# Performance work log

Hardware: AMD Instinct MI355X
Metric: run time of the kernel (lower is better)

The kernel has to match this reference:

```python
import jax, jax.numpy as jnp
import numpy as np

MARGIN = 0.2
NEG_FLOOR = 0.6


def setup_inputs() -> dict:
    key = jax.random.key(0)
    k1, k2 = jax.random.split(key)
    inputs_col = jax.random.normal(k1, (8192, 128), dtype=jnp.float32)
    targets_col = jax.random.randint(k2, (8192,), 0, 512, dtype=jnp.int64)
    return {"inputs_col": inputs_col, "targets_col": targets_col}


def reference(inputs_col, targets_col):
    n = inputs_col.shape[0]
    sim = inputs_col @ inputs_col.T  # [n, n]

    same = targets_col[:, None] == targets_col[None, :]
    eye = jnp.eye(n, dtype=bool)
    pos_mask = same & ~eye
    neg_mask = ~same

    has_pos = jnp.any(pos_mask, axis=1)  # rows with at least one positive pair

    neg_inf = jnp.float32(-jnp.inf)
    max_pos = jnp.max(jnp.where(pos_mask, sim, neg_inf), axis=1)  # pos_pair_[-1]
    max_neg = jnp.max(jnp.where(neg_mask, sim, neg_inf), axis=1)  # neg_pair_[-1]

    # positives with sim < max_neg + margin
    sel_pos = pos_mask & (sim < (max_neg + MARGIN)[:, None])
    # negatives with sim > max(0.6, max_pos) - margin
    neg_thresh = jnp.maximum(jnp.float32(NEG_FLOOR), max_pos) - MARGIN
    sel_neg = neg_mask & (sim > neg_thresh[:, None])

    pos_loss = jnp.sum(jnp.where(sel_pos, 1.0 - sim, 0.0), axis=1)
    neg_loss = jnp.sum(jnp.where(sel_neg, sim, 0.0), axis=1)

    row_loss = jnp.where(has_pos, pos_loss + neg_loss, 0.0)
    loss = jnp.sum(row_loss) / n

    # rows that contributed at least one selected negative (and had positives)
    neg_count = jnp.sum((jnp.any(sel_neg, axis=1) & has_pos).astype(jnp.int32))
    return loss, neg_count
```

## Files before the change

### kernel.cpp

```cpp
#include <hip/hip_runtime.h>
#include <hip/hip_bf16.h>

#define NPTS 8192
#define DDIM 128
#define MARGIN 0.2f
#define NEG_FLOOR 0.6f
#define SENT -1e30f
#define NCHUNK 16
#define CHUNK (NPTS / NCHUNK)
#define BM 128
#define JT 64
#define NSTEP (CHUNK / JT)
#define NRB (NPTS / 256)

typedef __attribute__((ext_vector_type(8))) short short8;
typedef __attribute__((ext_vector_type(4))) float f32x4;
typedef __attribute__((ext_vector_type(4))) unsigned int uint4v;
typedef __attribute__((ext_vector_type(4))) unsigned short ushort4v;


__device__ __forceinline__ unsigned short f2bf(unsigned u) {
    return (unsigned short)((u + 0x7FFFu + ((u >> 16) & 1u)) >> 16);
}

__global__ __launch_bounds__(256) void k_convert(const uint4v* __restrict__ x,
                                                 ushort4v* __restrict__ xb) {
    int i = blockIdx.x * 256 + threadIdx.x;
    uint4v u = x[i];
    ushort4v o;
    o.x = f2bf(u.x); o.y = f2bf(u.y); o.z = f2bf(u.z); o.w = f2bf(u.w);
    xb[i] = o;
}

__device__ __forceinline__ void gload16(const unsigned char* g, unsigned char* l) {
    __builtin_amdgcn_global_load_lds(
        (const __attribute__((address_space(1))) unsigned int*)(const void*)g,
        (__attribute__((address_space(3))) unsigned int*)(void*)l, 16, 0, 0);
}


#define MFMA_PAIR(B_, cg0_)                                                           \
    short8 bA0 = *(const short8*)((B_) + (cg0_)*4096 + 0 * 1024 + lane * 16);         \
    short8 bA1 = *(const short8*)((B_) + (cg0_)*4096 + 1 * 1024 + lane * 16);         \
    short8 bA2 = *(const short8*)((B_) + (cg0_)*4096 + 2 * 1024 + lane * 16);         \
    short8 bA3 = *(const short8*)((B_) + (cg0_)*4096 + 3 * 1024 + lane * 16);         \
    short8 bB0 = *(const short8*)((B_) + (cg0_)*4096 + 4096 + 0 * 1024 + lane * 16);  \
    short8 bB1 = *(const short8*)((B_) + (cg0_)*4096 + 4096 + 1 * 1024 + lane * 16);  \
    short8 bB2 = *(const short8*)((B_) + (cg0_)*4096 + 4096 + 2 * 1024 + lane * 16);  \
    short8 bB3 = *(const short8*)((B_) + (cg0_)*4096 + 4096 + 3 * 1024 + lane * 16);  \
    f32x4 accA0 = {0.f,0.f,0.f,0.f}, accA1 = {0.f,0.f,0.f,0.f};                       \
    f32x4 accB0 = {0.f,0.f,0.f,0.f}, accB1 = {0.f,0.f,0.f,0.f};                       \
    accA0 = __builtin_amdgcn_mfma_f32_16x16x32_bf16(a[0][0], bA0, accA0, 0, 0, 0);    \
    accA1 = __builtin_amdgcn_mfma_f32_16x16x32_bf16(a[1][0], bA0, accA1, 0, 0, 0);    \
    accB0 = __builtin_amdgcn_mfma_f32_16x16x32_bf16(a[0][0], bB0, accB0, 0, 0, 0);    \
    accB1 = __builtin_amdgcn_mfma_f32_16x16x32_bf16(a[1][0], bB0, accB1, 0, 0, 0);    \
    accA0 = __builtin_amdgcn_mfma_f32_16x16x32_bf16(a[0][1], bA1, accA0, 0, 0, 0);    \
    accA1 = __builtin_amdgcn_mfma_f32_16x16x32_bf16(a[1][1], bA1, accA1, 0, 0, 0);    \
    accB0 = __builtin_amdgcn_mfma_f32_16x16x32_bf16(a[0][1], bB1, accB0, 0, 0, 0);    \
    accB1 = __builtin_amdgcn_mfma_f32_16x16x32_bf16(a[1][1], bB1, accB1, 0, 0, 0);    \
    accA0 = __builtin_amdgcn_mfma_f32_16x16x32_bf16(a[0][2], bA2, accA0, 0, 0, 0);    \
    accA1 = __builtin_amdgcn_mfma_f32_16x16x32_bf16(a[1][2], bA2, accA1, 0, 0, 0);    \
    accB0 = __builtin_amdgcn_mfma_f32_16x16x32_bf16(a[0][2], bB2, accB0, 0, 0, 0);    \
    accB1 = __builtin_amdgcn_mfma_f32_16x16x32_bf16(a[1][2], bB2, accB1, 0, 0, 0);    \
    accA0 = __builtin_amdgcn_mfma_f32_16x16x32_bf16(a[0][3], bA3, accA0, 0, 0, 0);    \
    accA1 = __builtin_amdgcn_mfma_f32_16x16x32_bf16(a[1][3], bA3, accA1, 0, 0, 0);    \
    accB0 = __builtin_amdgcn_mfma_f32_16x16x32_bf16(a[0][3], bB3, accB0, 0, 0, 0);    \
    accB1 = __builtin_amdgcn_mfma_f32_16x16x32_bf16(a[1][3], bB3, accB1, 0, 0, 0);

__global__ __launch_bounds__(256, 2) void k_pass1(const unsigned short* __restrict__ xb,
                                                  const int* __restrict__ tg,
                                                  float* __restrict__ mp_part,
                                                  float* __restrict__ mn_part) {
    __shared__ __align__(16) unsigned char smB[JT * 256];
    __shared__ int ts[CHUNK];

    const unsigned char* xc = (const unsigned char*)xb;
    int tid  = threadIdx.x;
    int lane = tid & 63, w = tid >> 6, lr = lane & 15, hi = lane >> 4;
    int bb    = blockIdx.x;
    int chunk = bb & (NCHUNK - 1);
    int rb    = bb >> 4;
    int jbase = chunk * CHUNK;
    int rowbase = rb * BM + w * 32;

    ts[tid]       = tg[jbase + tid];
    ts[tid + 256] = tg[jbase + 256 + tid];

    short8 a[2][4];
#pragma unroll
    for (int rg = 0; rg < 2; ++rg)
#pragma unroll
        for (int ks = 0; ks < 4; ++ks)
            a[rg][ks] = *(const short8*)(xc + (size_t)(rowbase + rg * 16 + lr) * 256 + ks * 64 + hi * 16);

    int trow[2][4];
#pragma unroll
    for (int rg = 0; rg < 2; ++rg)
#pragma unroll
        for (int r = 0; r < 4; ++r)
            trow[rg][r] = tg[rowbase + rg * 16 + hi * 4 + r];

    float mp[2][4], mn[2][4];
#pragma unroll
    for (int rg = 0; rg < 2; ++rg)
#pragma unroll
        for (int r = 0; r < 4; ++r) { mp[rg][r] = SENT; mn[rg][r] = SENT; }

    for (int step = 0; step < NSTEP; ++step) {
        int j0 = jbase + step * JT;
        __syncthreads();
        const unsigned char* src = xc + (size_t)(j0 + w * 16 + lr) * 256 + hi * 16;
#pragma unroll
        for (int r = 0; r < 4; ++r)
            gload16(src + r * 64, smB + w * 4096 + r * 1024);
        __syncthreads();

        bool dstep = (unsigned)(rowbase - j0) < (unsigned)JT;
#pragma unroll
        for (int cgp = 0; cgp < 2; ++cgp) {
            int cg0 = cgp * 2;
            int tjA = ts[step * 64 + cg0 * 16 + lr];
            int tjB = ts[step * 64 + cg0 * 16 + 16 + lr];
            MFMA_PAIR(smB, cg0)
            if (dstep) {
#pragma unroll
                for (int rg = 0; rg < 2; ++rg) {
                    f32x4 aA = (rg == 0) ? accA0 : accA1;
                    f32x4 aB = (rg == 0) ? accB0 : accB1;
                    int base = rowbase + rg * 16 + hi * 4;
                    int dvA = j0 + cg0 * 16 + lr - base;
                    int dvB = dvA + 16;
#pragma unroll
                    for (int r = 0; r < 4; ++r) {
                        bool sA = (tjA == trow[rg][r]);
                        bool sB = (tjB == trow[rg][r]);
                        mp[rg][r] = fmaxf(mp[rg][r], (sA && dvA != r) ? aA[r] : SENT);
                        mn[rg][r] = fmaxf(mn[rg][r], sA ? SENT : aA[r]);
                        mp[rg][r] = fmaxf(mp[rg][r], (sB && dvB != r) ? aB[r] : SENT);
                        mn[rg][r] = fmaxf(mn[rg][r], sB ? SENT : aB[r]);
                    }
                }
            } else {
#pragma unroll
                for (int rg = 0; rg < 2; ++rg) {
                    f32x4 aA = (rg == 0) ? accA0 : accA1;
                    f32x4 aB = (rg == 0) ? accB0 : accB1;
#pragma unroll
                    for (int r = 0; r < 4; ++r) {
                        bool sA = (tjA == trow[rg][r]);
                        bool sB = (tjB == trow[rg][r]);
                        mp[rg][r] = fmaxf(mp[rg][r], sA ? aA[r] : SENT);
                        mn[rg][r] = fmaxf(mn[rg][r], sA ? SENT : aA[r]);
                        mp[rg][r] = fmaxf(mp[rg][r], sB ? aB[r] : SENT);
                        mn[rg][r] = fmaxf(mn[rg][r], sB ? SENT : aB[r]);
                    }
                }
            }
        }
    }

#pragma unroll
    for (int off = 1; off < 16; off <<= 1)
#pragma unroll
        for (int rg = 0; rg < 2; ++rg)
#pragma unroll
            for (int r = 0; r < 4; ++r) {
                mp[rg][r] = fmaxf(mp[rg][r], __shfl_xor(mp[rg][r], off, 64));
                mn[rg][r] = fmaxf(mn[rg][r], __shfl_xor(mn[rg][r], off, 64));
            }
    if (lr == 0) {
#pragma unroll
        for (int rg = 0; rg < 2; ++rg)
#pragma unroll
            for (int r = 0; r < 4; ++r) {
                int row = rowbase + rg * 16 + hi * 4 + r;
                mp_part[chunk * NPTS + row] = mp[rg][r];
                mn_part[chunk * NPTS + row] = mn[rg][r];
            }
    }
}

__global__ __launch_bounds__(256) void k_red1(const float* __restrict__ mp_part,
                                              const float* __restrict__ mn_part,
                                              float* __restrict__ maxpos,
                                              float* __restrict__ maxneg) {
    int row = blockIdx.x * 256 + threadIdx.x;
    float mp = SENT, mn = SENT;
#pragma unroll
    for (int c = 0; c < NCHUNK; ++c) {
        mp = fmaxf(mp, mp_part[c * NPTS + row]);
        mn = fmaxf(mn, mn_part[c * NPTS + row]);
    }
    maxpos[row] = mp;
    maxneg[row] = mn;
}

__global__ __launch_bounds__(256, 2) void k_pass2(const unsigned short* __restrict__ xb,
                                                  const int* __restrict__ tg,
                                                  const float* __restrict__ maxpos,
                                                  const float* __restrict__ maxneg,
                                                  float* __restrict__ sum_part,
                                                  int* __restrict__ flg_part) {
    __shared__ __align__(16) unsigned char smB[JT * 256];
    __shared__ int ts[CHUNK];

    const unsigned char* xc = (const unsigned char*)xb;
    int tid  = threadIdx.x;
    int lane = tid & 63, w = tid >> 6, lr = lane & 15, hi = lane >> 4;
    int bb    = blockIdx.x;
    int chunk = bb & (NCHUNK - 1);
    int rb    = bb >> 4;
    int jbase = chunk * CHUNK;
    int rowbase = rb * BM + w * 32;

    ts[tid]       = tg[jbase + tid];
    ts[tid + 256] = tg[jbase + 256 + tid];

    short8 a[2][4];
#pragma unroll
    for (int rg = 0; rg < 2; ++rg)
#pragma unroll
        for (int ks = 0; ks < 4; ++ks)
            a[rg][ks] = *(const short8*)(xc + (size_t)(rowbase + rg * 16 + lr) * 256 + ks * 64 + hi * 16);

    int trow[2][4];
    float pos_lim[2][4], neg_th[2][4];
#pragma unroll
    for (int rg = 0; rg < 2; ++rg)
#pragma unroll
        for (int r = 0; r < 4; ++r) {
            int row         = rowbase + rg * 16 + hi * 4 + r;
            trow[rg][r]     = tg[row];
            pos_lim[rg][r]  = maxneg[row] + MARGIN;
            neg_th[rg][r]   = fmaxf(NEG_FLOOR, maxpos[row]) - MARGIN;
        }

    float sumP[2][4] = {{0.f,0.f,0.f,0.f},{0.f,0.f,0.f,0.f}};
    float sumN[2][4] = {{0.f,0.f,0.f,0.f},{0.f,0.f,0.f,0.f}};

    for (int step = 0; step < NSTEP; ++step) {
        int j0 = jbase + step * JT;
        __syncthreads();
        const unsigned char* src = xc + (size_t)(j0 + w * 16 + lr) * 256 + hi * 16;
#pragma unroll
        for (int r = 0; r < 4; ++r)
            gload16(src + r * 64, smB + w * 4096 + r * 1024);
        __syncthreads();

        bool dstep = (unsigned)(rowbase - j0) < (unsigned)JT;
#pragma unroll
        for (int cgp = 0; cgp < 2; ++cgp) {
            int cg0 = cgp * 2;
            int tjA = ts[step * 64 + cg0 * 16 + lr];
            int tjB = ts[step * 64 + cg0 * 16 + 16 + lr];
            MFMA_PAIR(smB, cg0)
            if (dstep) {
#pragma unroll
                for (int rg = 0; rg < 2; ++rg) {
                    f32x4 aA = (rg == 0) ? accA0 : accA1;
                    f32x4 aB = (rg == 0) ? accB0 : accB1;
                    int base = rowbase + rg * 16 + hi * 4;
                    int dvA = j0 + cg0 * 16 + lr - base;
                    int dvB = dvA + 16;
#pragma unroll
                    for (int r = 0; r < 4; ++r) {
                        bool sA = (tjA == trow[rg][r]);
                        bool sB = (tjB == trow[rg][r]);
                        float vA = aA[r], vB = aB[r];
                        bool pA = sA && (dvA != r) && (vA < pos_lim[rg][r]);
                        bool nA = (!sA) && (vA > neg_th[rg][r]);
                        bool pB = sB && (dvB != r) && (vB < pos_lim[rg][r]);
                        bool nB = (!sB) && (vB > neg_th[rg][r]);
                        sumP[rg][r] += (pA ? (1.0f - vA) : 0.0f) + (pB ? (1.0f - vB) : 0.0f);
                        sumN[rg][r] += (nA ? vA : 0.0f) + (nB ? vB : 0.0f);
                    }
                }
            } else {
#pragma unroll
                for (int rg = 0; rg < 2; ++rg) {
                    f32x4 aA = (rg == 0) ? accA0 : accA1;
                    f32x4 aB = (rg == 0) ? accB0 : accB1;
#pragma unroll
                    for (int r = 0; r < 4; ++r) {
                        bool sA = (tjA == trow[rg][r]);
                        bool sB = (tjB == trow[rg][r]);
                        float vA = aA[r], vB = aB[r];
                        bool pA = sA && (vA < pos_lim[rg][r]);
                        bool nA = (!sA) && (vA > neg_th[rg][r]);
                        bool pB = sB && (vB < pos_lim[rg][r]);
                        bool nB = (!sB) && (vB > neg_th[rg][r]);
                        sumP[rg][r] += (pA ? (1.0f - vA) : 0.0f) + (pB ? (1.0f - vB) : 0.0f);
                        sumN[rg][r] += (nA ? vA : 0.0f) + (nB ? vB : 0.0f);
                    }
                }
            }
        }
    }

    float sum[2][4];
    int an = 0;
#pragma unroll
    for (int rg = 0; rg < 2; ++rg)
#pragma unroll
        for (int r = 0; r < 4; ++r) {
            sum[rg][r] = sumP[rg][r] + sumN[rg][r];
            an |= (sumN[rg][r] > 0.f) ? (1 << (rg * 4 + r)) : 0;
        }

#pragma unroll
    for (int off = 1; off < 16; off <<= 1) {
        an |= __shfl_xor(an, off, 64);
#pragma unroll
        for (int rg = 0; rg < 2; ++rg)
#pragma unroll
            for (int r = 0; r < 4; ++r)
                sum[rg][r] += __shfl_xor(sum[rg][r], off, 64);
    }
    if (lr == 0) {
#pragma unroll
        for (int rg = 0; rg < 2; ++rg)
#pragma unroll
            for (int r = 0; r < 4; ++r) {
                int row = rowbase + rg * 16 + hi * 4 + r;
                sum_part[chunk * NPTS + row] = sum[rg][r];
                flg_part[chunk * NPTS + row] = (an >> (rg * 4 + r)) & 1;
            }
    }
}

__global__ __launch_bounds__(256) void k_red2(const float* __restrict__ maxpos,
                                              const float* __restrict__ sum_part,
                                              const int* __restrict__ flg_part,
                                              float* __restrict__ blksum,
                                              float* __restrict__ blkcnt) {
    __shared__ float sf[256];
    __shared__ int   si[256];
    int t   = threadIdx.x;
    int row = blockIdx.x * 256 + t;

    bool hp = maxpos[row] > -1e29f;
    float rs = 0.f;
    int   fl = 0;
#pragma unroll
    for (int ch = 0; ch < NCHUNK; ++ch) {
        rs += sum_part[ch * NPTS + row];
        fl |= flg_part[ch * NPTS + row];
    }
    sf[t] = hp ? rs : 0.f;
    si[t] = (hp && fl) ? 1 : 0;
    __syncthreads();
    for (int off = 128; off > 0; off >>= 1) {
        if (t < off) { sf[t] += sf[t + off]; si[t] += si[t + off]; }
        __syncthreads();
    }
    if (t == 0) {
        blksum[blockIdx.x] = sf[0];
        blkcnt[blockIdx.x] = (float)si[0];
    }
}

__global__ __launch_bounds__(64) void k_final(const float* __restrict__ blksum,
                                              const float* __restrict__ blkcnt,
                                              float* __restrict__ out) {
    int t = threadIdx.x;
    float s = (t < NRB) ? blksum[t] : 0.f;
    float c = (t < NRB) ? blkcnt[t] : 0.f;
#pragma unroll
    for (int off = 32; off > 0; off >>= 1) {
        s += __shfl_xor(s, off, 64);
        c += __shfl_xor(c, off, 64);
    }
    if (t == 0) {
        out[0] = s / (float)NPTS;
        out[1] = c;
    }
}

extern "C" void kernel_launch(void* const* d_in, const int* in_sizes, int n_in,
                              void* d_out, int out_size, void* d_ws, size_t ws_size,
                              hipStream_t stream) {
    const float* x  = (const float*)d_in[0];
    const int*   tg = (const int*)d_in[1];
    float* out = (float*)d_out;

    unsigned short* xb = (unsigned short*)d_ws;
    char* base = (char*)d_ws + (size_t)NPTS * DDIM * 2;
    float* partA = (float*)(base);
    float* partB = (float*)(base + (size_t)NCHUNK * NPTS * 4);
    float* maxpos = (float*)(base + 2 * (size_t)NCHUNK * NPTS * 4);
    float* maxneg = (float*)(base + 2 * (size_t)NCHUNK * NPTS * 4 + NPTS * 4);
    float* blksum = (float*)(base + 2 * (size_t)NCHUNK * NPTS * 4 + 2 * NPTS * 4);
    float* blkcnt = blksum + NRB;

    k_convert<<<(NPTS * DDIM / 4) / 256, 256, 0, stream>>>((const uint4v*)x, (ushort4v*)xb);
    k_pass1<<<(NPTS / BM) * NCHUNK, 256, 0, stream>>>(xb, tg, partA, partB);
    k_red1<<<NPTS / 256, 256, 0, stream>>>(partA, partB, maxpos, maxneg);
    k_pass2<<<(NPTS / BM) * NCHUNK, 256, 0, stream>>>(xb, tg, maxpos, maxneg, partA, (int*)partB);
    k_red2<<<NRB, 256, 0, stream>>>(maxpos, partA, (const int*)partB, blksum, blkcnt);
    k_final<<<1, 64, 0, stream>>>(blksum, blkcnt, out);
}
```

Before: 76.57 us.

## Exploit symmetry of Gram matrix with upper-triangular panel tiling

Replaces the full row-block × column-chunk grid with a triangular grid of 128×128 panel pairs, so each off-diagonal tile of X·Xᵀ is computed once and contributes both row-wise and column-wise reductions (max pos/neg in pass 1, selected sums and flags in pass 2). Column reductions are done with cross-lane shuffles, combined across waves in shared memory and written to per-panel partial slots. This roughly halves MFMA work and operand loads. In exchange each block does extra column epilogue work and syncs, and the reduction kernels now read 64 slots instead of 16.

```diff
diff --git a/kernel.cpp b/kernel.cpp
--- a/kernel.cpp
+++ b/kernel.cpp
@@ -1,16 +1,18 @@
 #include <hip/hip_runtime.h>
 #include <hip/hip_bf16.h>
+#include <math.h>
 
 #define NPTS 8192
 #define DDIM 128
 #define MARGIN 0.2f
 #define NEG_FLOOR 0.6f
 #define SENT -1e30f
-#define NCHUNK 16
-#define CHUNK (NPTS / NCHUNK)
-#define BM 128
+#define NPAN 64
+#define PANR 128
 #define JT 64
-#define NSTEP (CHUNK / JT)
+#define NSTEP (PANR / JT)
+#define NSLOT NPAN
+#define NBLK (NPAN + NPAN * (NPAN - 1) / 2)
 #define NRB (NPTS / 256)
 
 typedef __attribute__((ext_vector_type(8))) short short8;
@@ -38,6 +40,24 @@
         (__attribute__((address_space(3))) unsigned int*)(void*)l, 16, 0, 0);
 }
 
+__device__ __forceinline__ void tri_map(int bb, int& pi, int& pj) {
+    if (bb < NPAN) { pi = bb; pj = bb; return; }
+    int t = bb - NPAN;
+    int J = (int)((1.0f + sqrtf(8.0f * (float)t + 1.0f)) * 0.5f);
+    while (J * (J - 1) / 2 > t) --J;
+    while (J * (J + 1) / 2 <= t) ++J;
+    pi = t - J * (J - 1) / 2;
+    pj = J;
+}
+
+#define STAGE_STEP                                                                    \
+    do {                                                                              \
+        const unsigned char* src_ = xc + (size_t)(j0 + w * 16 + lr) * 256 + hi * 16;  \
+        gload16(src_ + 0 * 64, smB + w * 4096 + 0 * 1024);                            \
+        gload16(src_ + 1 * 64, smB + w * 4096 + 1 * 1024);                            \
+        gload16(src_ + 2 * 64, smB + w * 4096 + 2 * 1024);                            \
+        gload16(src_ + 3 * 64, smB + w * 4096 + 3 * 1024);                            \
+    } while (0)
 
 #define MFMA_PAIR(B_, cg0_)                                                           \
     short8 bA0 = *(const short8*)((B_) + (cg0_)*4096 + 0 * 1024 + lane * 16);         \
@@ -72,19 +92,19 @@
                                                   float* __restrict__ mp_part,
                                                   float* __restrict__ mn_part) {
     __shared__ __align__(16) unsigned char smB[JT * 256];
-    __shared__ int ts[CHUNK];
+    __shared__ int   ts[PANR];
+    __shared__ float colP[4][64], colN[4][64];
 
     const unsigned char* xc = (const unsigned char*)xb;
     int tid  = threadIdx.x;
     int lane = tid & 63, w = tid >> 6, lr = lane & 15, hi = lane >> 4;
-    int bb    = blockIdx.x;
-    int chunk = bb & (NCHUNK - 1);
-    int rb    = bb >> 4;
-    int jbase = chunk * CHUNK;
-    int rowbase = rb * BM + w * 32;
-
-    ts[tid]       = tg[jbase + tid];
-    ts[tid + 256] = tg[jbase + 256 + tid];
+    int pi, pj;
+    tri_map(blockIdx.x, pi, pj);
+    bool diag = (pi == pj);
+    int jbase = pj * PANR;
+    int rowbase = pi * PANR + w * 32;
+
+    if (tid < PANR) ts[tid] = tg[jbase + tid];
 
     short8 a[2][4];
 #pragma unroll
@@ -109,20 +129,26 @@
     for (int step = 0; step < NSTEP; ++step) {
         int j0 = jbase + step * JT;
         __syncthreads();
-        const unsigned char* src = xc + (size_t)(j0 + w * 16 + lr) * 256 + hi * 16;
-#pragma unroll
-        for (int r = 0; r < 4; ++r)
-            gload16(src + r * 64, smB + w * 4096 + r * 1024);
+        if (!diag && step > 0 && tid < 128) {
+            int c = tid & 63;
+            int colg = jbase + (step - 1) * JT + c;
+            if (tid < 64)
+                mp_part[(size_t)pi * NPTS + colg] =
+                    fmaxf(fmaxf(colP[0][c], colP[1][c]), fmaxf(colP[2][c], colP[3][c]));
+            else
+                mn_part[(size_t)pi * NPTS + colg] =
+                    fmaxf(fmaxf(colN[0][c], colN[1][c]), fmaxf(colN[2][c], colN[3][c]));
+        }
+        STAGE_STEP;
         __syncthreads();
 
-        bool dstep = (unsigned)(rowbase - j0) < (unsigned)JT;
-#pragma unroll
-        for (int cgp = 0; cgp < 2; ++cgp) {
-            int cg0 = cgp * 2;
-            int tjA = ts[step * 64 + cg0 * 16 + lr];
-            int tjB = ts[step * 64 + cg0 * 16 + 16 + lr];
-            MFMA_PAIR(smB, cg0)
-            if (dstep) {
+        if (diag) {
+#pragma unroll
+            for (int cgp = 0; cgp < 2; ++cgp) {
+                int cg0 = cgp * 2;
+                int tjA = ts[step * 64 + cg0 * 16 + lr];
+                int tjB = ts[step * 64 + cg0 * 16 + 16 + lr];
+                MFMA_PAIR(smB, cg0)
 #pragma unroll
                 for (int rg = 0; rg < 2; ++rg) {
                     f32x4 aA = (rg == 0) ? accA0 : accA1;
@@ -140,7 +166,15 @@
                         mn[rg][r] = fmaxf(mn[rg][r], sB ? SENT : aB[r]);
                     }
                 }
-            } else {
+            }
+        } else {
+#pragma unroll
+            for (int cgp = 0; cgp < 2; ++cgp) {
+                int cg0 = cgp * 2;
+                int tjA = ts[step * 64 + cg0 * 16 + lr];
+                int tjB = ts[step * 64 + cg0 * 16 + 16 + lr];
+                MFMA_PAIR(smB, cg0)
+                float cpA = SENT, cnA = SENT, cpB = SENT, cnB = SENT;
 #pragma unroll
                 for (int rg = 0; rg < 2; ++rg) {
                     f32x4 aA = (rg == 0) ? accA0 : accA1;
@@ -149,14 +183,40 @@
                     for (int r = 0; r < 4; ++r) {
                         bool sA = (tjA == trow[rg][r]);
                         bool sB = (tjB == trow[rg][r]);
-                        mp[rg][r] = fmaxf(mp[rg][r], sA ? aA[r] : SENT);
-                        mn[rg][r] = fmaxf(mn[rg][r], sA ? SENT : aA[r]);
-                        mp[rg][r] = fmaxf(mp[rg][r], sB ? aB[r] : SENT);
-                        mn[rg][r] = fmaxf(mn[rg][r], sB ? SENT : aB[r]);
+                        float vpA = sA ? aA[r] : SENT, vnA = sA ? SENT : aA[r];
+                        float vpB = sB ? aB[r] : SENT, vnB = sB ? SENT : aB[r];
+                        mp[rg][r] = fmaxf(mp[rg][r], vpA);
+                        mn[rg][r] = fmaxf(mn[rg][r], vnA);
+                        mp[rg][r] = fmaxf(mp[rg][r], vpB);
+                        mn[rg][r] = fmaxf(mn[rg][r], vnB);
+                        cpA = fmaxf(cpA, vpA); cnA = fmaxf(cnA, vnA);
+                        cpB = fmaxf(cpB, vpB); cnB = fmaxf(cnB, vnB);
                     }
                 }
+                cpA = fmaxf(cpA, __shfl_xor(cpA, 16, 64)); cpA = fmaxf(cpA, __shfl_xor(cpA, 32, 64));
+                cnA = fmaxf(cnA, __shfl_xor(cnA, 16, 64)); cnA = fmaxf(cnA, __shfl_xor(cnA, 32, 64));
+                cpB = fmaxf(cpB, __shfl_xor(cpB, 16, 64)); cpB = fmaxf(cpB, __shfl_xor(cpB, 32, 64));
+                cnB = fmaxf(cnB, __shfl_xor(cnB, 16, 64)); cnB = fmaxf(cnB, __shfl_xor(cnB, 32, 64));
+                if (hi == 0) {
+                    colP[w][cg0 * 16 + lr]      = cpA;
+                    colN[w][cg0 * 16 + lr]      = cnA;
+                    colP[w][cg0 * 16 + 16 + lr] = cpB;
+                    colN[w][cg0 * 16 + 16 + lr] = cnB;
+                }
             }
         }
+    }
+
+    __syncthreads();
+    if (!diag && tid < 128) {
+        int c = tid & 63;
+        int colg = jbase + (NSTEP - 1) * JT + c;
+        if (tid < 64)
+            mp_part[(size_t)pi * NPTS + colg] =
+                fmaxf(fmaxf(colP[0][c], colP[1][c]), fmaxf(colP[2][c], colP[3][c]));
+        else
+            mn_part[(size_t)pi * NPTS + colg] =
+                fmaxf(fmaxf(colN[0][c], colN[1][c]), fmaxf(colN[2][c], colN[3][c]));
     }
 
 #pragma unroll
@@ -174,8 +234,8 @@
 #pragma unroll
             for (int r = 0; r < 4; ++r) {
                 int row = rowbase + rg * 16 + hi * 4 + r;
-                mp_part[chunk * NPTS + row] = mp[rg][r];
-                mn_part[chunk * NPTS + row] = mn[rg][r];
+                mp_part[(size_t)pj * NPTS + row] = mp[rg][r];
+                mn_part[(size_t)pj * NPTS + row] = mn[rg][r];
             }
     }
 }
@@ -187,9 +247,9 @@
     int row = blockIdx.x * 256 + threadIdx.x;
     float mp = SENT, mn = SENT;
 #pragma unroll
-    for (int c = 0; c < NCHUNK; ++c) {
-        mp = fmaxf(mp, mp_part[c * NPTS + row]);
-        mn = fmaxf(mn, mn_part[c * NPTS + row]);
+    for (int c = 0; c < NSLOT; ++c) {
+        mp = fmaxf(mp, mp_part[(size_t)c * NPTS + row]);
+        mn = fmaxf(mn, mn_part[(size_t)c * NPTS + row]);
     }
     maxpos[row] = mp;
     maxneg[row] = mn;
@@ -202,19 +262,25 @@
                                                   float* __restrict__ sum_part,
                                                   int* __restrict__ flg_part) {
     __shared__ __align__(16) unsigned char smB[JT * 256];
-    __shared__ int ts[CHUNK];
+    __shared__ int   ts[PANR];
+    __shared__ float plT[PANR], ntT[PANR];
+    __shared__ float colSP[4][64], colSN[4][64];
 
     const unsigned char* xc = (const unsigned char*)xb;
     int tid  = threadIdx.x;
     int lane = tid & 63, w = tid >> 6, lr = lane & 15, hi = lane >> 4;
-    int bb    = blockIdx.x;
-    int chunk = bb & (NCHUNK - 1);
-    int rb    = bb >> 4;
-    int jbase = chunk * CHUNK;
-    int rowbase = rb * BM + w * 32;
-
-    ts[tid]       = tg[jbase + tid];
-    ts[tid + 256] = tg[jbase + 256 + tid];
+    int pi, pj;
+    tri_map(blockIdx.x, pi, pj);
+    bool diag = (pi == pj);
+    int jbase = pj * PANR;
+    int rowbase = pi * PANR + w * 32;
+
+    if (tid < PANR) {
+        int c = jbase + tid;
+        ts[tid]  = tg[c];
+        plT[tid] = maxneg[c] + MARGIN;
+        ntT[tid] = fmaxf(NEG_FLOOR, maxpos[c]) - MARGIN;
+    }
 
     short8 a[2][4];
 #pragma unroll
@@ -229,10 +295,10 @@
     for (int rg = 0; rg < 2; ++rg)
 #pragma unroll
         for (int r = 0; r < 4; ++r) {
-            int row         = rowbase + rg * 16 + hi * 4 + r;
-            trow[rg][r]     = tg[row];
-            pos_lim[rg][r]  = maxneg[row] + MARGIN;
-            neg_th[rg][r]   = fmaxf(NEG_FLOOR, maxpos[row]) - MARGIN;
+            int row        = rowbase + rg * 16 + hi * 4 + r;
+            trow[rg][r]    = tg[row];
+            pos_lim[rg][r] = maxneg[row] + MARGIN;
+            neg_th[rg][r]  = fmaxf(NEG_FLOOR, maxpos[row]) - MARGIN;
         }
 
     float sumP[2][4] = {{0.f,0.f,0.f,0.f},{0.f,0.f,0.f,0.f}};
@@ -241,20 +307,24 @@
     for (int step = 0; step < NSTEP; ++step) {
         int j0 = jbase + step * JT;
         __syncthreads();
-        const unsigned char* src = xc + (size_t)(j0 + w * 16 + lr) * 256 + hi * 16;
-#pragma unroll
-        for (int r = 0; r < 4; ++r)
-            gload16(src + r * 64, smB + w * 4096 + r * 1024);
+        if (!diag && step > 0 && tid < 64) {
+            int c = tid;
+            int colg = jbase + (step - 1) * JT + c;
+            float SP = colSP[0][c] + colSP[1][c] + colSP[2][c] + colSP[3][c];
+            float SN = colSN[0][c] + colSN[1][c] + colSN[2][c] + colSN[3][c];
+            sum_part[(size_t)pi * NPTS + colg] = SP + SN;
+            flg_part[(size_t)pi * NPTS + colg] = (SN > 0.f) ? 1 : 0;
+        }
+        STAGE_STEP;
         __syncthreads();
 
-        bool dstep = (unsigned)(rowbase - j0) < (unsigned)JT;
-#pragma unroll
-        for (int cgp = 0; cgp < 2; ++cgp) {
-            int cg0 = cgp * 2;
-            int tjA = ts[step * 64 + cg0 * 16 + lr];
-            int tjB = ts[step * 64 + cg0 * 16 + 16 + lr];
-            MFMA_PAIR(smB, cg0)
-            if (dstep) {
+        if (diag) {
+#pragma unroll
+            for (int cgp = 0; cgp < 2; ++cgp) {
+                int cg0 = cgp * 2;
+                int tjA = ts[step * 64 + cg0 * 16 + lr];
+                int tjB = ts[step * 64 + cg0 * 16 + 16 + lr];
+                MFMA_PAIR(smB, cg0)
 #pragma unroll
                 for (int rg = 0; rg < 2; ++rg) {
                     f32x4 aA = (rg == 0) ? accA0 : accA1;
@@ -275,7 +345,18 @@
                         sumN[rg][r] += (nA ? vA : 0.0f) + (nB ? vB : 0.0f);
                     }
                 }
-            } else {
+            }
+        } else {
+#pragma unroll
+            for (int cgp = 0; cgp < 2; ++cgp) {
+                int cg0 = cgp * 2;
+                int idxA = step * 64 + cg0 * 16 + lr;
+                int idxB = idxA + 16;
+                int tjA = ts[idxA], tjB = ts[idxB];
+                float plA = plT[idxA], ntA = ntT[idxA];
+                float plB = plT[idxB], ntB = ntT[idxB];
+                MFMA_PAIR(smB, cg0)
+                float cpSA = 0.f, cnSA = 0.f, cpSB = 0.f, cnSB = 0.f;
 #pragma unroll
                 for (int rg = 0; rg < 2; ++rg) {
                     f32x4 aA = (rg == 0) ? accA0 : accA1;
@@ -291,10 +372,38 @@
                         bool nB = (!sB) && (vB > neg_th[rg][r]);
                         sumP[rg][r] += (pA ? (1.0f - vA) : 0.0f) + (pB ? (1.0f - vB) : 0.0f);
                         sumN[rg][r] += (nA ? vA : 0.0f) + (nB ? vB : 0.0f);
+                        bool pcA = sA && (vA < plA);
+                        bool ncA = (!sA) && (vA > ntA);
+                        bool pcB = sB && (vB < plB);
+                        bool ncB = (!sB) && (vB > ntB);
+                        cpSA += pcA ? (1.0f - vA) : 0.0f;
+                        cnSA += ncA ? vA : 0.0f;
+                        cpSB += pcB ? (1.0f - vB) : 0.0f;
+                        cnSB += ncB ? vB : 0.0f;
                     }
                 }
+                cpSA += __shfl_xor(cpSA, 16, 64); cpSA += __shfl_xor(cpSA, 32, 64);
+                cnSA += __shfl_xor(cnSA, 16, 64); cnSA += __shfl_xor(cnSA, 32, 64);
+                cpSB += __shfl_xor(cpSB, 16, 64); cpSB += __shfl_xor(cpSB, 32, 64);
+                cnSB += __shfl_xor(cnSB, 16, 64); cnSB += __shfl_xor(cnSB, 32, 64);
+                if (hi == 0) {
+                    colSP[w][cg0 * 16 + lr]      = cpSA;
+                    colSN[w][cg0 * 16 + lr]      = cnSA;
+                    colSP[w][cg0 * 16 + 16 + lr] = cpSB;
+                    colSN[w][cg0 * 16 + 16 + lr] = cnSB;
+                }
             }
         }
+    }
+
+    __syncthreads();
+    if (!diag && tid < 64) {
+        int c = tid;
+        int colg = jbase + (NSTEP - 1) * JT + c;
+        float SP = colSP[0][c] + colSP[1][c] + colSP[2][c] + colSP[3][c];
+        float SN = colSN[0][c] + colSN[1][c] + colSN[2][c] + colSN[3][c];
+        sum_part[(size_t)pi * NPTS + colg] = SP + SN;
+        flg_part[(size_t)pi * NPTS + colg] = (SN > 0.f) ? 1 : 0;
     }
 
     float sum[2][4];
@@ -322,8 +431,8 @@
 #pragma unroll
             for (int r = 0; r < 4; ++r) {
                 int row = rowbase + rg * 16 + hi * 4 + r;
-                sum_part[chunk * NPTS + row] = sum[rg][r];
-                flg_part[chunk * NPTS + row] = (an >> (rg * 4 + r)) & 1;
+                sum_part[(size_t)pj * NPTS + row] = sum[rg][r];
+                flg_part[(size_t)pj * NPTS + row] = (an >> (rg * 4 + r)) & 1;
             }
     }
 }
@@ -342,9 +451,9 @@
     float rs = 0.f;
     int   fl = 0;
 #pragma unroll
-    for (int ch = 0; ch < NCHUNK; ++ch) {
-        rs += sum_part[ch * NPTS + row];
-        fl |= flg_part[ch * NPTS + row];
+    for (int ch = 0; ch < NSLOT; ++ch) {
+        rs += sum_part[(size_t)ch * NPTS + row];
+        fl |= flg_part[(size_t)ch * NPTS + row];
     }
     sf[t] = hp ? rs : 0.f;
     si[t] = (hp && fl) ? 1 : 0;
@@ -386,16 +495,16 @@
     unsigned short* xb = (unsigned short*)d_ws;
     char* base = (char*)d_ws + (size_t)NPTS * DDIM * 2;
     float* partA = (float*)(base);
-    float* partB = (float*)(base + (size_t)NCHUNK * NPTS * 4);
-    float* maxpos = (float*)(base + 2 * (size_t)NCHUNK * NPTS * 4);
-    float* maxneg = (float*)(base + 2 * (size_t)NCHUNK * NPTS * 4 + NPTS * 4);
-    float* blksum = (float*)(base + 2 * (size_t)NCHUNK * NPTS * 4 + 2 * NPTS * 4);
+    float* partB = (float*)(base + (size_t)NSLOT * NPTS * 4);
+    float* maxpos = (float*)(base + 2 * (size_t)NSLOT * NPTS * 4);
+    float* maxneg = (float*)(base + 2 * (size_t)NSLOT * NPTS * 4 + NPTS * 4);
+    float* blksum = (float*)(base + 2 * (size_t)NSLOT * NPTS * 4 + 2 * NPTS * 4);
     float* blkcnt = blksum + NRB;
 
     k_convert<<<(NPTS * DDIM / 4) / 256, 256, 0, stream>>>((const uint4v*)x, (ushort4v*)xb);
-    k_pass1<<<(NPTS / BM) * NCHUNK, 256, 0, stream>>>(xb, tg, partA, partB);
+    k_pass1<<<NBLK, 256, 0, stream>>>(xb, tg, partA, partB);
     k_red1<<<NPTS / 256, 256, 0, stream>>>(partA, partB, maxpos, maxneg);
-    k_pass2<<<(NPTS / BM) * NCHUNK, 256, 0, stream>>>(xb, tg, maxpos, maxneg, partA, (int*)partB);
+    k_pass2<<<NBLK, 256, 0, stream>>>(xb, tg, maxpos, maxneg, partA, (int*)partB);
     k_red2<<<NRB, 256, 0, stream>>>(maxpos, partA, (const int*)partB, blksum, blkcnt);
     k_final<<<1, 64, 0, stream>>>(blksum, blkcnt, out);
 }
```

New measurement: 131.3 us. +71.4%, slower.
